# Performance work log

Hardware: AMD Instinct MI355X
Metric: run time of the kernel (lower is better)

Reference implementation:

```python
import jax, jax.numpy as jnp
import numpy as np

N_NODES = 100000
N_EDGES = 1000000
D_FEAT = 64
N_FILTER = 64
N_CLASSES = 16


def gcn_norm(edge_idx, n):
    """Add self-loops and compute symmetric normalization D^-1/2 (A+I) D^-1/2."""
    loop = jnp.arange(n, dtype=edge_idx.dtype)
    src = jnp.concatenate([edge_idx[0], loop])  # [E+N]
    dst = jnp.concatenate([edge_idx[1], loop])  # [E+N]
    w = jnp.ones(src.shape[0], dtype=jnp.float32)
    deg = jax.ops.segment_sum(w, dst, num_segments=n)  # in-degree incl. self-loop
    dinv = jnp.where(deg > 0, jax.lax.rsqrt(deg), 0.0)
    norm = dinv[src] * w * dinv[dst]  # [E+N]
    return src, dst, norm


def gcn_conv(x, W, b, src, dst, norm, n):
    h = x @ W                                   # [n, f] dense transform first (f <= d)
    msg = h[src] * norm[:, None]                # gather + scale  [E+N, f]
    out = jax.ops.segment_sum(msg, dst, num_segments=n)  # scatter-add  [n, f]
    return out + b


def setup_inputs() -> dict:
    key = jax.random.key(0)
    k1, k2, k3, k4 = jax.random.split(key, 4)
    X = jax.random.normal(k1, (N_NODES, D_FEAT), dtype=jnp.float32)
    edge_idx = jax.random.randint(k2, (2, N_EDGES), 0, N_NODES, dtype=jnp.int64)
    W1 = jax.random.normal(k3, (D_FEAT, N_FILTER), dtype=jnp.float32) * 0.05
    b1 = jnp.zeros((N_FILTER,), dtype=jnp.float32)
    W2 = jax.random.normal(k4, (N_FILTER, N_CLASSES), dtype=jnp.float32) * 0.05
    b2 = jnp.zeros((N_CLASSES,), dtype=jnp.float32)
    return {"X": X, "edge_idx": edge_idx, "W1": W1, "b1": b1, "W2": W2, "b2": b2}


def reference(X, edge_idx, W1, b1, W2, b2):
    n = X.shape[0]
    src, dst, norm = gcn_norm(edge_idx, n)
    x = gcn_conv(X, W1, b1, src, dst, norm, n)
    x = jax.nn.relu(x)
    # dropout p=0 -> identity
    x = gcn_conv(x, W2, b2, src, dst, norm, n)
    return x  # raw logits; pred_layer is not applied in the torch forward
```

## Files before the change

kernel.cpp:

```cpp
#include <hip/hip_runtime.h>
#include <hip/hip_bf16.h>


constexpr int N = 100000;
constexpr int E = 1000000;
constexpr int NB = (N + 511) / 512;
constexpr int CAP = 6144;
constexpr int CSTRIDE = 32;
constexpr int CHUNK = 2048;
constexpr int NBLK = (E + CHUNK - 1) / CHUNK;

__device__ __forceinline__ float rl_f(float v, int lane) {
    return __int_as_float(__builtin_amdgcn_readlane(__float_as_int(v), lane));
}
__device__ __forceinline__ int rl_i(int v, int lane) {
    return __builtin_amdgcn_readlane(v, lane);
}

__global__ void k_bfill(const int* __restrict__ src, const int* __restrict__ dst,
                        int* __restrict__ cursor, int* __restrict__ bkt) {
    __shared__ int hist[256];
    __shared__ int lbase[256];
    __shared__ int gbase[256];
    __shared__ int lcur[256];
    __shared__ int stage[CHUNK];
    __shared__ unsigned char sbkt[CHUNK];
    int t = threadIdx.x;
    int e0 = blockIdx.x * CHUNK;
    int cnt = min(CHUNK, E - e0);

    hist[t] = 0;
    __syncthreads();
    for (int j = t; j < cnt; j += 256)
        atomicAdd(&hist[dst[e0 + j] >> 9], 1);
    __syncthreads();
    int h = hist[t];
    lbase[t] = h;
    __syncthreads();
    for (int off = 1; off < 256; off <<= 1) {
        int x = (t >= off) ? lbase[t - off] : 0;
        __syncthreads();
        lbase[t] += x;
        __syncthreads();
    }
    int excl = lbase[t] - h;
    __syncthreads();
    lbase[t] = excl;
    lcur[t] = 0;
    if (t < NB) gbase[t] = h ? atomicAdd(&cursor[t * CSTRIDE], h) : 0;
    __syncthreads();
    for (int j = t; j < cnt; j += 256) {
        int d = dst[e0 + j];
        int b = d >> 9;
        int pos = lbase[b] + atomicAdd(&lcur[b], 1);
        stage[pos] = ((d & 511) << 17) | src[e0 + j];
        sbkt[pos] = (unsigned char)b;
    }
    __syncthreads();
    for (int j = t; j < cnt; j += 256) {
        int b = sbkt[j];
        int gpos = gbase[b] + (j - lbase[b]);
        if (gpos < CAP) bkt[b * CAP + gpos] = stage[j];
    }
}

__global__ void k_bscan(const int* __restrict__ cursor, int* __restrict__ bucket_base,
                        int* __restrict__ row_ptr) {
    __shared__ int sd[256];
    int t = threadIdx.x;
    int c = (t < NB) ? cursor[t * CSTRIDE] : 0;
    sd[t] = c;
    __syncthreads();
    for (int off = 1; off < 256; off <<= 1) {
        int x = (t >= off) ? sd[t - off] : 0;
        __syncthreads();
        sd[t] += x;
        __syncthreads();
    }
    if (t < NB) bucket_base[t] = sd[t] - c;
    if (t == 0) row_ptr[N] = E;
}

__global__ void k_bfine(const int* __restrict__ cursor, const int* __restrict__ bucket_base,
                        const int* __restrict__ bkt, int* __restrict__ row_ptr,
                        float* __restrict__ dinv, int* __restrict__ csr_src) {
    __shared__ int cnt[512];
    __shared__ int excl[512];
    __shared__ int s2[256];
    int b = blockIdx.x;
    int t = threadIdx.x;
    int m = cursor[b * CSTRIDE];
    int base = bucket_base[b];
    const int* bb = bkt + b * CAP;
    cnt[t] = 0; cnt[t + 256] = 0;
    __syncthreads();
    for (int j = t; j < m; j += 256) atomicAdd(&cnt[bb[j] >> 17], 1);
    __syncthreads();
    int pairSum = cnt[2 * t] + cnt[2 * t + 1];
    s2[t] = pairSum;
    __syncthreads();
    for (int off = 1; off < 256; off <<= 1) {
        int x = (t >= off) ? s2[t - off] : 0;
        __syncthreads();
        s2[t] += x;
        __syncthreads();
    }
    int exclPair = s2[t] - pairSum;
    excl[2 * t] = exclPair;
    excl[2 * t + 1] = exclPair + cnt[2 * t];
    __syncthreads();
#pragma unroll
    for (int hh = 0; hh < 2; ++hh) {
        int k = t + hh * 256;
        int node = b * 512 + k;
        if (node < N) {
            row_ptr[node] = base + excl[k];
            dinv[node] = rsqrtf((float)(cnt[k] + 1));
        }
    }
    __syncthreads();
    for (int j = t; j < m; j += 256) {
        int v = bb[j];
        int p = atomicAdd(&excl[v >> 17], 1);
        csr_src[base + p] = v & 0x1FFFF;
    }
}

__global__ void k_gemm1(const float* __restrict__ X, const float* __restrict__ W1,
                        const float* __restrict__ dinv, __hip_bfloat16* __restrict__ h1s) {
    int t = threadIdx.x;
    int lane = t & 63;
    int wid = (blockIdx.x * 256 + t) >> 6;
    float w1[64];
#pragma unroll
    for (int k = 0; k < 64; ++k) w1[k] = W1[k * 64 + lane];
    for (int row = wid; row < N; row += 4096) {
        float x = X[(size_t)row * 64 + lane];
        float acc = 0.f;
#pragma unroll
        for (int k = 0; k < 64; ++k) acc = fmaf(rl_f(x, k), w1[k], acc);
        h1s[(size_t)row * 64 + lane] = __float2bfloat16(acc * dinv[row]);
    }
}

__global__ void k_layer12(const int* __restrict__ row_ptr, const int* __restrict__ csr_src,
                          const float* __restrict__ dinv, const __hip_bfloat16* __restrict__ h1s,
                          const float* __restrict__ b1, const float* __restrict__ W2,
                          __hip_bfloat16* __restrict__ h2s) {
    int t = threadIdx.x;
    int lane = t & 63;
    int g = lane >> 4, c = lane & 15;
    int wid = (blockIdx.x * 256 + t) >> 6;
    float w2[16];
#pragma unroll
    for (int j = 0; j < 16; ++j) w2[j] = W2[(g * 16 + j) * 16 + c];
    float b1v = b1[lane];

    for (int d = wid; d < N; d += 8192) {
        int rp0 = row_ptr[d], rp1 = row_ptr[d + 1];
        float dv = dinv[d];
        float a0 = __bfloat162float(h1s[(size_t)d * 64 + lane]);
        float a1 = 0.f, a2 = 0.f, a3 = 0.f;
        for (int base = rp0; base < rp1; base += 64) {
            int nloc = min(64, rp1 - base);
            int sidx = (lane < nloc) ? csr_src[base + lane] : 0;
            int j = 0;
            for (; j + 3 < nloc; j += 4) {
                int s0 = rl_i(sidx, j), s1 = rl_i(sidx, j + 1);
                int s2v = rl_i(sidx, j + 2), s3 = rl_i(sidx, j + 3);
                a0 += __bfloat162float(h1s[(size_t)s0 * 64 + lane]);
                a1 += __bfloat162float(h1s[(size_t)s1 * 64 + lane]);
                a2 += __bfloat162float(h1s[(size_t)s2v * 64 + lane]);
                a3 += __bfloat162float(h1s[(size_t)s3 * 64 + lane]);
            }
            for (; j < nloc; ++j)
                a0 += __bfloat162float(h1s[(size_t)rl_i(sidx, j) * 64 + lane]);
        }
        float y = fmaxf(dv * ((a0 + a1) + (a2 + a3)) + b1v, 0.f);
        float o = 0.f;
#pragma unroll
        for (int j = 0; j < 16; ++j) o = fmaf(__shfl(y, (lane & 48) | j), w2[j], o);
        o += __shfl_xor(o, 16);
        o += __shfl_xor(o, 32);
        if (lane < 16) h2s[(size_t)d * 16 + lane] = __float2bfloat16(o * dv);
    }
}

__global__ void k_gather2(const int* __restrict__ row_ptr, const int* __restrict__ csr_src,
                          const float* __restrict__ dinv, const __hip_bfloat16* __restrict__ h2s,
                          const float* __restrict__ b2, float* __restrict__ out) {
    int t = threadIdx.x;
    int lane = t & 63;
    int g = lane >> 4, c = lane & 15;
    int d = blockIdx.x * 4 + (t >> 6);
    int rp0 = row_ptr[d], rp1 = row_ptr[d + 1];
    float dv = dinv[d];
    float acc = (g == 0) ? __bfloat162float(h2s[(size_t)d * 16 + c]) : 0.f;
    for (int j = rp0 + g; j < rp1; j += 4) {
        int s = csr_src[j];
        acc += __bfloat162float(h2s[(size_t)s * 16 + c]);
    }
    acc += __shfl_xor(acc, 16);
    acc += __shfl_xor(acc, 32);
    if (lane < 16) out[(size_t)d * 16 + c] = dv * acc + b2[c];
}

extern "C" void kernel_launch(void* const* d_in, const int* in_sizes, int n_in,
                              void* d_out, int out_size, void* d_ws, size_t ws_size,
                              hipStream_t stream) {
    const float* X  = (const float*)d_in[0];
    const int*   ei = (const int*)d_in[1];
    const float* W1 = (const float*)d_in[2];
    const float* b1 = (const float*)d_in[3];
    const float* W2 = (const float*)d_in[4];
    const float* b2 = (const float*)d_in[5];
    float* out = (float*)d_out;

    int* cursor      = (int*)d_ws;
    int* bucket_base = cursor + NB * CSTRIDE;
    int* row_ptr     = bucket_base + NB;
    int* bkt         = row_ptr + N + 1;
    int* csr_src     = bkt + NB * CAP;
    float* dinv      = (float*)(csr_src + E);
    __hip_bfloat16* h1s = (__hip_bfloat16*)(dinv + N);
    __hip_bfloat16* h2s = h1s + (size_t)N * 64;

    const int* src = ei;
    const int* dst = ei + E;

    hipMemsetAsync(cursor, 0, NB * CSTRIDE * sizeof(int), stream);
    k_bfill<<<NBLK, 256, 0, stream>>>(src, dst, cursor, bkt);
    k_bscan<<<1, 256, 0, stream>>>(cursor, bucket_base, row_ptr);
    k_bfine<<<NB, 256, 0, stream>>>(cursor, bucket_base, bkt, row_ptr, dinv, csr_src);
    k_gemm1<<<1024, 256, 0, stream>>>(X, W1, dinv, h1s);
    k_layer12<<<2048, 256, 0, stream>>>(row_ptr, csr_src, dinv, h1s, b1, W2, h2s);
    k_gather2<<<N / 4, 256, 0, stream>>>(row_ptr, csr_src, dinv, h2s, b2, out);
}
```

Baseline: 219.4 us.

## Vectorize bf16 gathers, fuse bucket scan into fine sort, pack stores

The layer-1 gather now has each 16-lane quarter of a wave fetch a different neighbor row with 8-byte loads holding 4 bf16 values. Partial sums are combined by shuffles and redistributed to lanes before the W2 projection. The second gather uses 4-byte loads over 8 edge groups, and h1s/h2s/out stores are packed into pairs. The separate bucket-scan kernel is folded into every k_bfine block, which each redo the 256-entry scan, removing one launch at the cost of redundant work and extra shuffles.

```diff
diff --git a/kernel.cpp b/kernel.cpp
--- a/kernel.cpp
+++ b/kernel.cpp
@@ -10,12 +10,14 @@
 constexpr int CHUNK = 2048;
 constexpr int NBLK = (E + CHUNK - 1) / CHUNK;
 
-__device__ __forceinline__ float rl_f(float v, int lane) {
-    return __int_as_float(__builtin_amdgcn_readlane(__float_as_int(v), lane));
-}
-__device__ __forceinline__ int rl_i(int v, int lane) {
-    return __builtin_amdgcn_readlane(v, lane);
-}
+__device__ __forceinline__ float rl_f(float v, int l) {
+    return __int_as_float(__builtin_amdgcn_readlane(__float_as_int(v), l));
+}
+__device__ __forceinline__ int rl_i(int v, int l) {
+    return __builtin_amdgcn_readlane(v, l);
+}
+__device__ __forceinline__ float bflo(unsigned u) { return __uint_as_float(u << 16); }
+__device__ __forceinline__ float bfhi(unsigned u) { return __uint_as_float(u & 0xffff0000u); }
 
 __global__ void k_bfill(const int* __restrict__ src, const int* __restrict__ dst,
                         int* __restrict__ cursor, int* __restrict__ bkt) {
@@ -64,33 +66,27 @@
     }
 }
 
-__global__ void k_bscan(const int* __restrict__ cursor, int* __restrict__ bucket_base,
-                        int* __restrict__ row_ptr) {
+__global__ void k_bfine(const int* __restrict__ cursor, const int* __restrict__ bkt,
+                        int* __restrict__ row_ptr, float* __restrict__ dinv,
+                        int* __restrict__ csr_src) {
     __shared__ int sd[256];
-    int t = threadIdx.x;
-    int c = (t < NB) ? cursor[t * CSTRIDE] : 0;
-    sd[t] = c;
-    __syncthreads();
-    for (int off = 1; off < 256; off <<= 1) {
-        int x = (t >= off) ? sd[t - off] : 0;
-        __syncthreads();
-        sd[t] += x;
-        __syncthreads();
-    }
-    if (t < NB) bucket_base[t] = sd[t] - c;
-    if (t == 0) row_ptr[N] = E;
-}
-
-__global__ void k_bfine(const int* __restrict__ cursor, const int* __restrict__ bucket_base,
-                        const int* __restrict__ bkt, int* __restrict__ row_ptr,
-                        float* __restrict__ dinv, int* __restrict__ csr_src) {
     __shared__ int cnt[512];
     __shared__ int excl[512];
     __shared__ int s2[256];
     int b = blockIdx.x;
     int t = threadIdx.x;
+    int c = (t < NB) ? cursor[t * CSTRIDE] : 0;
+    sd[t] = c;
+    __syncthreads();
+    for (int off = 1; off < 256; off <<= 1) {
+        int x = (t >= off) ? sd[t - off] : 0;
+        __syncthreads();
+        sd[t] += x;
+        __syncthreads();
+    }
     int m = cursor[b * CSTRIDE];
-    int base = bucket_base[b];
+    int base = sd[b] - m;
+    if (b == 0 && t == 0) row_ptr[N] = E;
     const int* bb = bkt + b * CAP;
     cnt[t] = 0; cnt[t + 256] = 0;
     __syncthreads();
@@ -139,7 +135,14 @@
         float acc = 0.f;
 #pragma unroll
         for (int k = 0; k < 64; ++k) acc = fmaf(rl_f(x, k), w1[k], acc);
-        h1s[(size_t)row * 64 + lane] = __float2bfloat16(acc * dinv[row]);
+        acc *= dinv[row];
+        float up = __shfl_xor(acc, 1);
+        if (!(lane & 1)) {
+            __hip_bfloat162 p;
+            p.x = __float2bfloat16(acc);
+            p.y = __float2bfloat16(up);
+            *(__hip_bfloat162*)(h1s + (size_t)row * 64 + lane) = p;
+        }
     }
 }
 
@@ -149,40 +152,66 @@
                           __hip_bfloat16* __restrict__ h2s) {
     int t = threadIdx.x;
     int lane = t & 63;
-    int g = lane >> 4, c = lane & 15;
+    int g = lane >> 4;
+    int q = lane & 15;
     int wid = (blockIdx.x * 256 + t) >> 6;
     float w2[16];
 #pragma unroll
-    for (int j = 0; j < 16; ++j) w2[j] = W2[(g * 16 + j) * 16 + c];
+    for (int j = 0; j < 16; ++j) w2[j] = W2[(g * 16 + j) * 16 + q];
     float b1v = b1[lane];
+    const uint2* H = (const uint2*)h1s;
 
     for (int d = wid; d < N; d += 8192) {
         int rp0 = row_ptr[d], rp1 = row_ptr[d + 1];
         float dv = dinv[d];
-        float a0 = __bfloat162float(h1s[(size_t)d * 64 + lane]);
-        float a1 = 0.f, a2 = 0.f, a3 = 0.f;
+        float a0 = 0.f, a1 = 0.f, a2 = 0.f, a3 = 0.f;
+        if (g == 0) {
+            uint2 u = H[(size_t)d * 16 + q];
+            a0 = bflo(u.x); a1 = bfhi(u.x); a2 = bflo(u.y); a3 = bfhi(u.y);
+        }
         for (int base = rp0; base < rp1; base += 64) {
             int nloc = min(64, rp1 - base);
             int sidx = (lane < nloc) ? csr_src[base + lane] : 0;
             int j = 0;
             for (; j + 3 < nloc; j += 4) {
                 int s0 = rl_i(sidx, j), s1 = rl_i(sidx, j + 1);
-                int s2v = rl_i(sidx, j + 2), s3 = rl_i(sidx, j + 3);
-                a0 += __bfloat162float(h1s[(size_t)s0 * 64 + lane]);
-                a1 += __bfloat162float(h1s[(size_t)s1 * 64 + lane]);
-                a2 += __bfloat162float(h1s[(size_t)s2v * 64 + lane]);
-                a3 += __bfloat162float(h1s[(size_t)s3 * 64 + lane]);
+                int s2v = rl_i(sidx, j + 2), s3v = rl_i(sidx, j + 3);
+                int sa = (lane & 16) ? s1 : s0;
+                int sb = (lane & 16) ? s3v : s2v;
+                int sg = (lane & 32) ? sb : sa;
+                uint2 u = H[(size_t)sg * 16 + q];
+                a0 += bflo(u.x); a1 += bfhi(u.x); a2 += bflo(u.y); a3 += bfhi(u.y);
             }
-            for (; j < nloc; ++j)
-                a0 += __bfloat162float(h1s[(size_t)rl_i(sidx, j) * 64 + lane]);
-        }
-        float y = fmaxf(dv * ((a0 + a1) + (a2 + a3)) + b1v, 0.f);
+            for (; j < nloc; ++j) {
+                int s = rl_i(sidx, j);
+                if (lane < 16) {
+                    uint2 u = H[(size_t)s * 16 + q];
+                    a0 += bflo(u.x); a1 += bfhi(u.x); a2 += bflo(u.y); a3 += bfhi(u.y);
+                }
+            }
+        }
+        a0 += __shfl_xor(a0, 16); a1 += __shfl_xor(a1, 16);
+        a2 += __shfl_xor(a2, 16); a3 += __shfl_xor(a3, 16);
+        a0 += __shfl_xor(a0, 32); a1 += __shfl_xor(a1, 32);
+        a2 += __shfl_xor(a2, 32); a3 += __shfl_xor(a3, 32);
+        int srcl = lane >> 2;
+        float v0 = __shfl(a0, srcl), v1 = __shfl(a1, srcl);
+        float v2 = __shfl(a2, srcl), v3 = __shfl(a3, srcl);
+        float ysum = (lane & 2) ? ((lane & 1) ? v3 : v2) : ((lane & 1) ? v1 : v0);
+        float y = fmaxf(fmaf(dv, ysum, b1v), 0.f);
         float o = 0.f;
 #pragma unroll
         for (int j = 0; j < 16; ++j) o = fmaf(__shfl(y, (lane & 48) | j), w2[j], o);
         o += __shfl_xor(o, 16);
         o += __shfl_xor(o, 32);
-        if (lane < 16) h2s[(size_t)d * 16 + lane] = __float2bfloat16(o * dv);
+        o *= dv;
+        float oup = __shfl_xor(o, 1);
+        if (lane < 16 && !(lane & 1)) {
+            __hip_bfloat162 p;
+            p.x = __float2bfloat16(o);
+            p.y = __float2bfloat16(oup);
+            *(__hip_bfloat162*)(h2s + (size_t)d * 16 + lane) = p;
+        }
     }
 }
 
@@ -191,18 +220,31 @@
                           const float* __restrict__ b2, float* __restrict__ out) {
     int t = threadIdx.x;
     int lane = t & 63;
-    int g = lane >> 4, c = lane & 15;
+    int g = lane >> 3;
+    int cp = lane & 7;
     int d = blockIdx.x * 4 + (t >> 6);
     int rp0 = row_ptr[d], rp1 = row_ptr[d + 1];
     float dv = dinv[d];
-    float acc = (g == 0) ? __bfloat162float(h2s[(size_t)d * 16 + c]) : 0.f;
-    for (int j = rp0 + g; j < rp1; j += 4) {
+    const unsigned* H2 = (const unsigned*)h2s;
+    float e0 = 0.f, e1 = 0.f;
+    if (g == 0) {
+        unsigned u = H2[(size_t)d * 8 + cp];
+        e0 = bflo(u); e1 = bfhi(u);
+    }
+    for (int j = rp0 + g; j < rp1; j += 8) {
         int s = csr_src[j];
-        acc += __bfloat162float(h2s[(size_t)s * 16 + c]);
-    }
-    acc += __shfl_xor(acc, 16);
-    acc += __shfl_xor(acc, 32);
-    if (lane < 16) out[(size_t)d * 16 + c] = dv * acc + b2[c];
+        unsigned u = H2[(size_t)s * 8 + cp];
+        e0 += bflo(u); e1 += bfhi(u);
+    }
+    e0 += __shfl_xor(e0, 8);  e1 += __shfl_xor(e1, 8);
+    e0 += __shfl_xor(e0, 16); e1 += __shfl_xor(e1, 16);
+    e0 += __shfl_xor(e0, 32); e1 += __shfl_xor(e1, 32);
+    if (lane < 8) {
+        float2 r;
+        r.x = fmaf(dv, e0, b2[2 * cp]);
+        r.y = fmaf(dv, e1, b2[2 * cp + 1]);
+        *(float2*)(out + (size_t)d * 16 + 2 * cp) = r;
+    }
 }
 
 extern "C" void kernel_launch(void* const* d_in, const int* in_sizes, int n_in,
@@ -216,12 +258,11 @@
     const float* b2 = (const float*)d_in[5];
     float* out = (float*)d_out;
 
-    int* cursor      = (int*)d_ws;
-    int* bucket_base = cursor + NB * CSTRIDE;
-    int* row_ptr     = bucket_base + NB;
-    int* bkt         = row_ptr + N + 1;
-    int* csr_src     = bkt + NB * CAP;
-    float* dinv      = (float*)(csr_src + E);
+    int* cursor  = (int*)d_ws;
+    int* row_ptr = cursor + NB * CSTRIDE;
+    int* bkt     = row_ptr + N + 4;
+    int* csr_src = bkt + NB * CAP;
+    float* dinv  = (float*)(csr_src + E);
     __hip_bfloat16* h1s = (__hip_bfloat16*)(dinv + N);
     __hip_bfloat16* h2s = h1s + (size_t)N * 64;
 
@@ -230,8 +271,7 @@
 
     hipMemsetAsync(cursor, 0, NB * CSTRIDE * sizeof(int), stream);
     k_bfill<<<NBLK, 256, 0, stream>>>(src, dst, cursor, bkt);
-    k_bscan<<<1, 256, 0, stream>>>(cursor, bucket_base, row_ptr);
-    k_bfine<<<NB, 256, 0, stream>>>(cursor, bucket_base, bkt, row_ptr, dinv, csr_src);
+    k_bfine<<<NB, 256, 0, stream>>>(cursor, bkt, row_ptr, dinv, csr_src);
     k_gemm1<<<1024, 256, 0, stream>>>(X, W1, dinv, h1s);
     k_layer12<<<2048, 256, 0, stream>>>(row_ptr, csr_src, dinv, h1s, b1, W2, h2s);
     k_gather2<<<N / 4, 256, 0, stream>>>(row_ptr, csr_src, dinv, h2s, b2, out);
```

New measurement: 217.2 us. No clear change (-1.0%).
